# Optimization experiments

Hardware: AMD Instinct MI355X
Metric: run time of the kernel (lower is better)

Reference implementation:

```python
import jax, jax.numpy as jnp
import numpy as np
from jax import lax

START_IDX = 0
END_IDX = 1
NEG = -10000.0


def setup_inputs() -> dict:
    key = jax.random.key(0)
    k_h, k_t = jax.random.split(key)
    seq_len, tagset_size = 8192, 2048
    h = jax.random.normal(k_h, (seq_len, tagset_size), dtype=jnp.float32)
    transitions = jax.random.normal(k_t, (tagset_size, tagset_size), dtype=jnp.float32)
    # CRF constraints: nothing transitions FROM end into start row; nothing transitions TO end col
    transitions = transitions.at[START_IDX, :].set(NEG)
    transitions = transitions.at[:, END_IDX].set(NEG)
    return {"h": h, "transitions": transitions}


def reference(h, transitions):
    # h: [S, T] emission scores; transitions: [T, T], transitions[i, j] = score(j -> i)
    T = transitions.shape[0]
    init = jnp.full((T,), NEG, dtype=h.dtype).at[START_IDX].set(0.0)

    def step(forward_var, emit):
        # scores[i, j] = forward_var[j] + transitions[i, j] + emit[i]
        scores = forward_var[None, :] + transitions + emit[:, None]  # [T, T]
        return jax.nn.logsumexp(scores, axis=-1), None

    forward_var, _ = lax.scan(step, init, h)
    terminal = forward_var + transitions[END_IDX]
    return jax.nn.logsumexp(terminal)
```

## Files before the change

kernel.cpp:

```cpp
#include <hip/hip_runtime.h>


#define TSZ   2048
#define NCH   16
#define GBLK  16
#define NW    8
#define CH_LEN 512
#define BURN  24
#define START_I 0
#define END_I   1

typedef float v4f __attribute__((ext_vector_type(4)));
typedef _Float16 h2f __attribute__((ext_vector_type(2)));

__device__ __forceinline__ h2f pk16(float a, float b) {
    return __builtin_bit_cast(h2f, __builtin_amdgcn_cvt_pkrtz(a, b));
}
__device__ __forceinline__ void st_coh(float* p, float v) {
    asm volatile("global_store_dword %0, %1, off sc0 sc1"
                 :: "v"(p), "v"(v) : "memory");
}
__device__ __forceinline__ float ld_coh1(const float* p) {
    float r;
    asm volatile("global_load_dword %0, %1, off sc0 sc1\n\ts_waitcnt vmcnt(0)"
                 : "=&v"(r) : "v"(p) : "memory");
    return r;
}
__device__ __forceinline__ v4f ld_coh4(const float* p) {
    v4f r;
    asm volatile("global_load_dwordx4 %0, %1, off sc0 sc1\n\ts_waitcnt vmcnt(0)"
                 : "=&v"(r) : "v"(p) : "memory");
    return r;
}

__global__ __launch_bounds__(512, 1)
void crf_chain(const float* __restrict__ h, const float* __restrict__ tr,
               float* __restrict__ out, float* __restrict__ ws)
{
    const int tid  = threadIdx.x;
    const int lane = tid & 63;
    const int wv   = tid >> 6;
    const int blk  = blockIdx.x;
    const int c    = blk >> 4;
    const int b    = blk & (GBLK - 1);
    const int row_base = b * 128 + wv * 16;

    float* u_bufs = ws;
    float* usave  = ws + NCH * 2 * TSZ;
    float* ufin   = usave + NCH * TSZ;
    float* cbuf   = ufin + NCH * TSZ;
    int*   posts  = (int*)((char*)ws + 524544);

    __shared__ unsigned long long els64[32][512];
    __shared__ unsigned long long uh_sh[512];

    h2f e2r[12][16];
    #pragma unroll
    for (int r = 0; r < 12; ++r) {
        const float* trow = tr + (size_t)(row_base + r) * TSZ + 4 * lane;
        #pragma unroll
        for (int k = 0; k < 8; ++k) {
            float4 t4 = *(const float4*)(trow + 256 * k);
            e2r[r][2 * k]     = pk16(__expf(t4.x), __expf(t4.y));
            e2r[r][2 * k + 1] = pk16(__expf(t4.z), __expf(t4.w));
        }
    }
    #pragma unroll
    for (int rr = 0; rr < 4; ++rr) {
        const float* trow = tr + (size_t)(row_base + 12 + rr) * TSZ + 4 * lane;
        #pragma unroll
        for (int k = 0; k < 8; ++k) {
            float4 t4 = *(const float4*)(trow + 256 * k);
            unsigned lo = __builtin_bit_cast(unsigned, pk16(__expf(t4.x), __expf(t4.y)));
            unsigned hi = __builtin_bit_cast(unsigned, pk16(__expf(t4.z), __expf(t4.w)));
            els64[wv * 4 + rr][lane + 64 * k] =
                ((unsigned long long)hi << 32) | (unsigned long long)lo;
        }
    }

    const int s_keep  = c * CH_LEN;
    const int s_begin = (c == 0) ? 0 : (s_keep - BURN);
    const int s_end   = s_keep + CH_LEN;
    const int T_iter  = s_end - s_begin;

    const int q    = ((lane & 1) << 2) | (lane & 2) | ((lane >> 2) & 1);
    const int grow = row_base + q;

    if (tid < 128) {
        int row = b * 128 + tid;
        float v = (c == 0) ? ((row == START_I) ? 1.0f : 0.0f) : 1.0f;
        st_coh(&u_bufs[(c * 2 + 0) * TSZ + row], v);
    }
    __syncthreads();

    float Chat = 0.0f;

    for (int t = 0; t < T_iter; ++t) {
        const int s = s_begin + t;
        float* u_out = u_bufs + (c * 2 + ((t + 1) & 1)) * TSZ;
        const int out_neg = ((t + 1) >> 1) & 1;

        float hv0 = 0.0f, hv1 = 0.0f;
        if (lane < 8) {
            hv0 = h[(size_t)s * TSZ + grow];
            hv1 = h[(size_t)s * TSZ + grow + 8];
        }

        if (wv == 0) {
            const float* u_in = u_bufs + (c * 2 + (t & 1)) * TSZ;
            const int in_neg  = (t >> 1) & 1;

            v4f u0, u1, u2, u3, u4, u5, u6, u7;
            const float* pa = u_in + 4 * lane;
            const float* pb = pa + 1024;
            for (;;) {
                asm volatile(
                    "global_load_dwordx4 %0, %8, off sc0 sc1\n\t"
                    "global_load_dwordx4 %1, %8, off offset:1024 sc0 sc1\n\t"
                    "global_load_dwordx4 %2, %8, off offset:2048 sc0 sc1\n\t"
                    "global_load_dwordx4 %3, %8, off offset:3072 sc0 sc1\n\t"
                    "global_load_dwordx4 %4, %9, off sc0 sc1\n\t"
                    "global_load_dwordx4 %5, %9, off offset:1024 sc0 sc1\n\t"
                    "global_load_dwordx4 %6, %9, off offset:2048 sc0 sc1\n\t"
                    "global_load_dwordx4 %7, %9, off offset:3072 sc0 sc1\n\t"
                    "s_waitcnt vmcnt(0)"
                    : "=&v"(u0), "=&v"(u1), "=&v"(u2), "=&v"(u3),
                      "=&v"(u4), "=&v"(u5), "=&v"(u6), "=&v"(u7)
                    : "v"(pa), "v"(pb)
                    : "memory");
                bool fresh;
                if (in_neg) {
                    int a = __float_as_int(u0.x) & __float_as_int(u0.y) & __float_as_int(u0.z) & __float_as_int(u0.w);
                    a &= __float_as_int(u1.x) & __float_as_int(u1.y) & __float_as_int(u1.z) & __float_as_int(u1.w);
                    a &= __float_as_int(u2.x) & __float_as_int(u2.y) & __float_as_int(u2.z) & __float_as_int(u2.w);
                    a &= __float_as_int(u3.x) & __float_as_int(u3.y) & __float_as_int(u3.z) & __float_as_int(u3.w);
                    a &= __float_as_int(u4.x) & __float_as_int(u4.y) & __float_as_int(u4.z) & __float_as_int(u4.w);
                    a &= __float_as_int(u5.x) & __float_as_int(u5.y) & __float_as_int(u5.z) & __float_as_int(u5.w);
                    a &= __float_as_int(u6.x) & __float_as_int(u6.y) & __float_as_int(u6.z) & __float_as_int(u6.w);
                    a &= __float_as_int(u7.x) & __float_as_int(u7.y) & __float_as_int(u7.z) & __float_as_int(u7.w);
                    fresh = (a < 0);
                } else {
                    int o = __float_as_int(u0.x) | __float_as_int(u0.y) | __float_as_int(u0.z) | __float_as_int(u0.w);
                    o |= __float_as_int(u1.x) | __float_as_int(u1.y) | __float_as_int(u1.z) | __float_as_int(u1.w);
                    o |= __float_as_int(u2.x) | __float_as_int(u2.y) | __float_as_int(u2.z) | __float_as_int(u2.w);
                    o |= __float_as_int(u3.x) | __float_as_int(u3.y) | __float_as_int(u3.z) | __float_as_int(u3.w);
                    o |= __float_as_int(u4.x) | __float_as_int(u4.y) | __float_as_int(u4.z) | __float_as_int(u4.w);
                    o |= __float_as_int(u5.x) | __float_as_int(u5.y) | __float_as_int(u5.z) | __float_as_int(u5.w);
                    o |= __float_as_int(u6.x) | __float_as_int(u6.y) | __float_as_int(u6.z) | __float_as_int(u6.w);
                    o |= __float_as_int(u7.x) | __float_as_int(u7.y) | __float_as_int(u7.z) | __float_as_int(u7.w);
                    fresh = (o >= 0);
                }
                if (__all(fresh)) break;
            }

            float m;
            m =          fmaxf(fmaxf(fabsf(u0.x), fabsf(u0.y)), fmaxf(fabsf(u0.z), fabsf(u0.w)));
            m = fmaxf(m, fmaxf(fmaxf(fabsf(u1.x), fabsf(u1.y)), fmaxf(fabsf(u1.z), fabsf(u1.w))));
            m = fmaxf(m, fmaxf(fmaxf(fabsf(u2.x), fabsf(u2.y)), fmaxf(fabsf(u2.z), fabsf(u2.w))));
            m = fmaxf(m, fmaxf(fmaxf(fabsf(u3.x), fabsf(u3.y)), fmaxf(fabsf(u3.z), fabsf(u3.w))));
            m = fmaxf(m, fmaxf(fmaxf(fabsf(u4.x), fabsf(u4.y)), fmaxf(fabsf(u4.z), fabsf(u4.w))));
            m = fmaxf(m, fmaxf(fmaxf(fabsf(u5.x), fabsf(u5.y)), fmaxf(fabsf(u5.z), fabsf(u5.w))));
            m = fmaxf(m, fmaxf(fmaxf(fabsf(u6.x), fabsf(u6.y)), fmaxf(fabsf(u6.z), fabsf(u6.w))));
            m = fmaxf(m, fmaxf(fmaxf(fabsf(u7.x), fabsf(u7.y)), fmaxf(fabsf(u7.z), fabsf(u7.w))));
            #pragma unroll
            for (int d = 1; d < 64; d <<= 1) m = fmaxf(m, __shfl_xor(m, d, 64));

            const float rn = (in_neg ? -1.0f : 1.0f) / m;
            h2f uh[16];
            uh[0]  = pk16(u0.x * rn, u0.y * rn);  uh[1]  = pk16(u0.z * rn, u0.w * rn);
            uh[2]  = pk16(u1.x * rn, u1.y * rn);  uh[3]  = pk16(u1.z * rn, u1.w * rn);
            uh[4]  = pk16(u2.x * rn, u2.y * rn);  uh[5]  = pk16(u2.z * rn, u2.w * rn);
            uh[6]  = pk16(u3.x * rn, u3.y * rn);  uh[7]  = pk16(u3.z * rn, u3.w * rn);
            uh[8]  = pk16(u4.x * rn, u4.y * rn);  uh[9]  = pk16(u4.z * rn, u4.w * rn);
            uh[10] = pk16(u5.x * rn, u5.y * rn);  uh[11] = pk16(u5.z * rn, u5.w * rn);
            uh[12] = pk16(u6.x * rn, u6.y * rn);  uh[13] = pk16(u6.z * rn, u6.w * rn);
            uh[14] = pk16(u7.x * rn, u7.y * rn);  uh[15] = pk16(u7.z * rn, u7.w * rn);
            #pragma unroll
            for (int k = 0; k < 8; ++k) {
                unsigned long long qw =
                    ((unsigned long long)__builtin_bit_cast(unsigned, uh[2 * k + 1]) << 32) |
                    (unsigned long long)__builtin_bit_cast(unsigned, uh[2 * k]);
                uh_sh[lane + 64 * k] = qw;
            }

            if ((s + 1) > s_keep) Chat += __logf(m);
        }

        __syncthreads();

        h2f uh[16];
        #pragma unroll
        for (int k = 0; k < 8; ++k) {
            unsigned long long qw = uh_sh[lane + 64 * k];
            uh[2 * k]     = __builtin_bit_cast(h2f, (unsigned)qw);
            uh[2 * k + 1] = __builtin_bit_cast(h2f, (unsigned)(qw >> 32));
        }

        float acc[8];
        #pragma unroll
        for (int r = 0; r < 8; ++r) acc[r] = 0.0f;
        #pragma unroll
        for (int k = 0; k < 16; ++k) {
            #pragma unroll
            for (int r = 0; r < 8; ++r)
                acc[r] = __builtin_amdgcn_fdot2(e2r[r][k], uh[k], acc[r], false);
        }
        #pragma unroll
        for (int r = 0; r < 4; ++r) {
            float send = (lane & 1) ? acc[r] : acc[r + 4];
            float recv = __shfl_xor(send, 1, 64);
            float keep = (lane & 1) ? acc[r + 4] : acc[r];
            acc[r] = keep + recv;
        }
        #pragma unroll
        for (int r = 0; r < 2; ++r) {
            float send = (lane & 2) ? acc[r] : acc[r + 2];
            float recv = __shfl_xor(send, 2, 64);
            float keep = (lane & 2) ? acc[r + 2] : acc[r];
            acc[r] = keep + recv;
        }
        {
            float send = (lane & 4) ? acc[0] : acc[1];
            float recv = __shfl_xor(send, 4, 64);
            float keep = (lane & 4) ? acc[1] : acc[0];
            acc[0] = keep + recv;
        }
        acc[0] += __shfl_xor(acc[0], 8, 64);
        acc[0] += __shfl_xor(acc[0], 16, 64);
        acc[0] += __shfl_xor(acc[0], 32, 64);
        float resA = acc[0];

        #pragma unroll
        for (int r = 0; r < 8; ++r) acc[r] = 0.0f;
        #pragma unroll
        for (int k = 0; k < 8; ++k) {
            unsigned long long q0 = els64[wv * 4 + 0][lane + 64 * k];
            unsigned long long q1 = els64[wv * 4 + 1][lane + 64 * k];
            unsigned long long q2 = els64[wv * 4 + 2][lane + 64 * k];
            unsigned long long q3 = els64[wv * 4 + 3][lane + 64 * k];
            #pragma unroll
            for (int r = 0; r < 4; ++r) {
                acc[r] = __builtin_amdgcn_fdot2(e2r[8 + r][2 * k],     uh[2 * k],     acc[r], false);
                acc[r] = __builtin_amdgcn_fdot2(e2r[8 + r][2 * k + 1], uh[2 * k + 1], acc[r], false);
            }
            acc[4] = __builtin_amdgcn_fdot2(__builtin_bit_cast(h2f, (unsigned)q0),         uh[2 * k],     acc[4], false);
            acc[4] = __builtin_amdgcn_fdot2(__builtin_bit_cast(h2f, (unsigned)(q0 >> 32)), uh[2 * k + 1], acc[4], false);
            acc[5] = __builtin_amdgcn_fdot2(__builtin_bit_cast(h2f, (unsigned)q1),         uh[2 * k],     acc[5], false);
            acc[5] = __builtin_amdgcn_fdot2(__builtin_bit_cast(h2f, (unsigned)(q1 >> 32)), uh[2 * k + 1], acc[5], false);
            acc[6] = __builtin_amdgcn_fdot2(__builtin_bit_cast(h2f, (unsigned)q2),         uh[2 * k],     acc[6], false);
            acc[6] = __builtin_amdgcn_fdot2(__builtin_bit_cast(h2f, (unsigned)(q2 >> 32)), uh[2 * k + 1], acc[6], false);
            acc[7] = __builtin_amdgcn_fdot2(__builtin_bit_cast(h2f, (unsigned)q3),         uh[2 * k],     acc[7], false);
            acc[7] = __builtin_amdgcn_fdot2(__builtin_bit_cast(h2f, (unsigned)(q3 >> 32)), uh[2 * k + 1], acc[7], false);
        }
        #pragma unroll
        for (int r = 0; r < 4; ++r) {
            float send = (lane & 1) ? acc[r] : acc[r + 4];
            float recv = __shfl_xor(send, 1, 64);
            float keep = (lane & 1) ? acc[r + 4] : acc[r];
            acc[r] = keep + recv;
        }
        #pragma unroll
        for (int r = 0; r < 2; ++r) {
            float send = (lane & 2) ? acc[r] : acc[r + 2];
            float recv = __shfl_xor(send, 2, 64);
            float keep = (lane & 2) ? acc[r + 2] : acc[r];
            acc[r] = keep + recv;
        }
        {
            float send = (lane & 4) ? acc[0] : acc[1];
            float recv = __shfl_xor(send, 4, 64);
            float keep = (lane & 4) ? acc[1] : acc[0];
            acc[0] = keep + recv;
        }
        acc[0] += __shfl_xor(acc[0], 8, 64);
        acc[0] += __shfl_xor(acc[0], 16, 64);
        acc[0] += __shfl_xor(acc[0], 32, 64);
        float resB = acc[0];

        if (lane < 8) {
            float utA = resA * __expf(hv0);
            float utB = resB * __expf(hv1);
            st_coh(&u_out[grow],     out_neg ? -utA : utA);
            st_coh(&u_out[grow + 8], out_neg ? -utB : utB);
            if (c > 0 && (s + 1) == s_keep) {
                st_coh(&usave[c * TSZ + grow],     utA);
                st_coh(&usave[c * TSZ + grow + 8], utB);
            }
            if ((s + 1) == s_end) {
                st_coh(&ufin[c * TSZ + grow],     utA);
                st_coh(&ufin[c * TSZ + grow + 8], utB);
            }
        }
    }

    if (b == 0 && wv == 0 && lane == 0) st_coh(&cbuf[c], Chat);
    asm volatile("s_waitcnt vmcnt(0)" ::: "memory");
    if (lane == 0)
        __hip_atomic_store(&posts[blk * NW + wv], 1,
                           __ATOMIC_RELAXED, __HIP_MEMORY_SCOPE_AGENT);

    if (c == 0 && b == 0 && wv == 0) {
        int ok;
        do {
            __builtin_amdgcn_s_sleep(1);
            ok = 1;
            #pragma unroll
            for (int i = 0; i < 32; ++i) {
                int v = __hip_atomic_load(&posts[lane + 64 * i],
                                          __ATOMIC_RELAXED, __HIP_MEMORY_SCOPE_AGENT);
                ok &= (v == 1);
            }
        } while (!__all(ok));

        float O = 0.0f;
        for (int cc = 1; cc < NCH; ++cc) {
            float sa = 0.0f, sb = 0.0f;
            for (int j = 4 * lane; j < TSZ; j += 256) {
                v4f a4 = ld_coh4(&ufin[(cc - 1) * TSZ + j]);
                v4f b4 = ld_coh4(&usave[cc * TSZ + j]);
                sa += a4.x + a4.y + a4.z + a4.w;
                sb += b4.x + b4.y + b4.z + b4.w;
            }
            #pragma unroll
            for (int d = 1; d < 64; d <<= 1) {
                sa += __shfl_xor(sa, d, 64);
                sb += __shfl_xor(sb, d, 64);
            }
            O += ld_coh1(&cbuf[cc - 1]) + __logf(sa) - __logf(sb);
        }
        float se = 0.0f;
        for (int j = 4 * lane; j < TSZ; j += 256) {
            const float4 t4 = *(const float4*)(tr + (size_t)END_I * TSZ + j);
            v4f uf = ld_coh4(&ufin[(NCH - 1) * TSZ + j]);
            se += __expf(t4.x) * uf.x + __expf(t4.y) * uf.y +
                  __expf(t4.z) * uf.z + __expf(t4.w) * uf.w;
        }
        #pragma unroll
        for (int d = 1; d < 64; d <<= 1) se += __shfl_xor(se, d, 64);

        float ans = O + ld_coh1(&cbuf[NCH - 1]) + __logf(se);
        if (lane == 0) out[0] = ans;
    }
}

extern "C" void kernel_launch(void* const* d_in, const int* in_sizes, int n_in,
                              void* d_out, int out_size, void* d_ws, size_t ws_size,
                              hipStream_t stream) {
    const float* h  = (const float*)d_in[0];
    const float* tr = (const float*)d_in[1];
    (void)in_sizes; (void)n_in; (void)out_size; (void)ws_size;
    crf_chain<<<dim3(NCH * GBLK), dim3(512), 0, stream>>>(h, tr, (float*)d_out, (float*)d_ws);
}
```

Baseline: 2.227 ms.

## Interleave four sequence chunks per block group to hide inter-block polling latency

Splits the sequence into 64 chunks of 128 steps instead of 16 chunks of 512. Each group of 16 blocks now advances four chunks round-robin: it polls one chunk's state vector, packs another and runs the GEMV for a third in the same phase. The poll-and-normalize work is spread across all eight waves, with a shared-memory max reduction, instead of sitting on wave 0. The aim is to overlap the cross-block publish and poll latency of the serial recurrence with useful compute. In exchange it adds four times as many burn-in segments, more shared memory and more complex phase bookkeeping.

```diff
diff --git a/kernel.cpp b/kernel.cpp
--- a/kernel.cpp
+++ b/kernel.cpp
@@ -2,11 +2,12 @@
 
 
 #define TSZ   2048
-#define NCH   16
+#define NCH   64
 #define GBLK  16
 #define NW    8
-#define CH_LEN 512
+#define CH_LEN 128
 #define BURN  24
+#define TCYC  (CH_LEN + BURN)
 #define START_I 0
 #define END_I   1
 
@@ -41,7 +42,7 @@
     const int lane = tid & 63;
     const int wv   = tid >> 6;
     const int blk  = blockIdx.x;
-    const int c    = blk >> 4;
+    const int g    = blk >> 4;
     const int b    = blk & (GBLK - 1);
     const int row_base = b * 128 + wv * 16;
 
@@ -49,10 +50,11 @@
     float* usave  = ws + NCH * 2 * TSZ;
     float* ufin   = usave + NCH * TSZ;
     float* cbuf   = ufin + NCH * TSZ;
-    int*   posts  = (int*)((char*)ws + 524544);
+    int*   posts  = (int*)((char*)ws + 2097408);
 
     __shared__ unsigned long long els64[32][512];
-    __shared__ unsigned long long uh_sh[512];
+    __shared__ unsigned long long uh_sh[4][512];
+    __shared__ float smax_sh[4][8] __attribute__((aligned(16)));
 
     h2f e2r[12][16];
     #pragma unroll
@@ -78,124 +80,78 @@
         }
     }
 
-    const int s_keep  = c * CH_LEN;
-    const int s_begin = (c == 0) ? 0 : (s_keep - BURN);
-    const int s_end   = s_keep + CH_LEN;
-    const int T_iter  = s_end - s_begin;
+    const int ccs[4] = { g, 16 + g, 32 + g, 48 + g };
+    int s0s[4], sks[4], ses[4];
+    float* ubs[4];
+    #pragma unroll
+    for (int r = 0; r < 4; ++r) {
+        sks[r] = ccs[r] * CH_LEN;
+        ses[r] = sks[r] + CH_LEN;
+        s0s[r] = (ccs[r] == 0) ? 0 : (sks[r] - BURN);
+        ubs[r] = u_bufs + ccs[r] * 2 * TSZ;
+    }
 
     const int q    = ((lane & 1) << 2) | (lane & 2) | ((lane >> 2) & 1);
     const int grow = row_base + q;
 
     if (tid < 128) {
         int row = b * 128 + tid;
-        float v = (c == 0) ? ((row == START_I) ? 1.0f : 0.0f) : 1.0f;
-        st_coh(&u_bufs[(c * 2 + 0) * TSZ + row], v);
+        #pragma unroll
+        for (int r = 0; r < 4; ++r)
+            st_coh(&ubs[r][row],
+                   (ccs[r] == 0) ? ((row == START_I) ? 1.0f : 0.0f) : 1.0f);
     }
     __syncthreads();
 
-    float Chat = 0.0f;
-
-    for (int t = 0; t < T_iter; ++t) {
-        const int s = s_begin + t;
-        float* u_out = u_bufs + (c * 2 + ((t + 1) & 1)) * TSZ;
-        const int out_neg = ((t + 1) >> 1) & 1;
-
-        float hv0 = 0.0f, hv1 = 0.0f;
-        if (lane < 8) {
-            hv0 = h[(size_t)s * TSZ + grow];
-            hv1 = h[(size_t)s * TSZ + grow + 8];
-        }
-
-        if (wv == 0) {
-            const float* u_in = u_bufs + (c * 2 + (t & 1)) * TSZ;
-            const int in_neg  = (t >> 1) & 1;
-
-            v4f u0, u1, u2, u3, u4, u5, u6, u7;
-            const float* pa = u_in + 4 * lane;
-            const float* pb = pa + 1024;
-            for (;;) {
-                asm volatile(
-                    "global_load_dwordx4 %0, %8, off sc0 sc1\n\t"
-                    "global_load_dwordx4 %1, %8, off offset:1024 sc0 sc1\n\t"
-                    "global_load_dwordx4 %2, %8, off offset:2048 sc0 sc1\n\t"
-                    "global_load_dwordx4 %3, %8, off offset:3072 sc0 sc1\n\t"
-                    "global_load_dwordx4 %4, %9, off sc0 sc1\n\t"
-                    "global_load_dwordx4 %5, %9, off offset:1024 sc0 sc1\n\t"
-                    "global_load_dwordx4 %6, %9, off offset:2048 sc0 sc1\n\t"
-                    "global_load_dwordx4 %7, %9, off offset:3072 sc0 sc1\n\t"
-                    "s_waitcnt vmcnt(0)"
-                    : "=&v"(u0), "=&v"(u1), "=&v"(u2), "=&v"(u3),
-                      "=&v"(u4), "=&v"(u5), "=&v"(u6), "=&v"(u7)
-                    : "v"(pa), "v"(pb)
-                    : "memory");
-                bool fresh;
-                if (in_neg) {
-                    int a = __float_as_int(u0.x) & __float_as_int(u0.y) & __float_as_int(u0.z) & __float_as_int(u0.w);
-                    a &= __float_as_int(u1.x) & __float_as_int(u1.y) & __float_as_int(u1.z) & __float_as_int(u1.w);
-                    a &= __float_as_int(u2.x) & __float_as_int(u2.y) & __float_as_int(u2.z) & __float_as_int(u2.w);
-                    a &= __float_as_int(u3.x) & __float_as_int(u3.y) & __float_as_int(u3.z) & __float_as_int(u3.w);
-                    a &= __float_as_int(u4.x) & __float_as_int(u4.y) & __float_as_int(u4.z) & __float_as_int(u4.w);
-                    a &= __float_as_int(u5.x) & __float_as_int(u5.y) & __float_as_int(u5.z) & __float_as_int(u5.w);
-                    a &= __float_as_int(u6.x) & __float_as_int(u6.y) & __float_as_int(u6.z) & __float_as_int(u6.w);
-                    a &= __float_as_int(u7.x) & __float_as_int(u7.y) & __float_as_int(u7.z) & __float_as_int(u7.w);
-                    fresh = (a < 0);
-                } else {
-                    int o = __float_as_int(u0.x) | __float_as_int(u0.y) | __float_as_int(u0.z) | __float_as_int(u0.w);
-                    o |= __float_as_int(u1.x) | __float_as_int(u1.y) | __float_as_int(u1.z) | __float_as_int(u1.w);
-                    o |= __float_as_int(u2.x) | __float_as_int(u2.y) | __float_as_int(u2.z) | __float_as_int(u2.w);
-                    o |= __float_as_int(u3.x) | __float_as_int(u3.y) | __float_as_int(u3.z) | __float_as_int(u3.w);
-                    o |= __float_as_int(u4.x) | __float_as_int(u4.y) | __float_as_int(u4.z) | __float_as_int(u4.w);
-                    o |= __float_as_int(u5.x) | __float_as_int(u5.y) | __float_as_int(u5.z) | __float_as_int(u5.w);
-                    o |= __float_as_int(u6.x) | __float_as_int(u6.y) | __float_as_int(u6.z) | __float_as_int(u6.w);
-                    o |= __float_as_int(u7.x) | __float_as_int(u7.y) | __float_as_int(u7.z) | __float_as_int(u7.w);
-                    fresh = (o >= 0);
-                }
-                if (__all(fresh)) break;
-            }
-
-            float m;
-            m =          fmaxf(fmaxf(fabsf(u0.x), fabsf(u0.y)), fmaxf(fabsf(u0.z), fabsf(u0.w)));
-            m = fmaxf(m, fmaxf(fmaxf(fabsf(u1.x), fabsf(u1.y)), fmaxf(fabsf(u1.z), fabsf(u1.w))));
-            m = fmaxf(m, fmaxf(fmaxf(fabsf(u2.x), fabsf(u2.y)), fmaxf(fabsf(u2.z), fabsf(u2.w))));
-            m = fmaxf(m, fmaxf(fmaxf(fabsf(u3.x), fabsf(u3.y)), fmaxf(fabsf(u3.z), fabsf(u3.w))));
-            m = fmaxf(m, fmaxf(fmaxf(fabsf(u4.x), fabsf(u4.y)), fmaxf(fabsf(u4.z), fabsf(u4.w))));
-            m = fmaxf(m, fmaxf(fmaxf(fabsf(u5.x), fabsf(u5.y)), fmaxf(fabsf(u5.z), fabsf(u5.w))));
-            m = fmaxf(m, fmaxf(fmaxf(fabsf(u6.x), fabsf(u6.y)), fmaxf(fabsf(u6.z), fabsf(u6.w))));
-            m = fmaxf(m, fmaxf(fmaxf(fabsf(u7.x), fabsf(u7.y)), fmaxf(fabsf(u7.z), fabsf(u7.w))));
-            #pragma unroll
-            for (int d = 1; d < 64; d <<= 1) m = fmaxf(m, __shfl_xor(m, d, 64));
-
-            const float rn = (in_neg ? -1.0f : 1.0f) / m;
-            h2f uh[16];
-            uh[0]  = pk16(u0.x * rn, u0.y * rn);  uh[1]  = pk16(u0.z * rn, u0.w * rn);
-            uh[2]  = pk16(u1.x * rn, u1.y * rn);  uh[3]  = pk16(u1.z * rn, u1.w * rn);
-            uh[4]  = pk16(u2.x * rn, u2.y * rn);  uh[5]  = pk16(u2.z * rn, u2.w * rn);
-            uh[6]  = pk16(u3.x * rn, u3.y * rn);  uh[7]  = pk16(u3.z * rn, u3.w * rn);
-            uh[8]  = pk16(u4.x * rn, u4.y * rn);  uh[9]  = pk16(u4.z * rn, u4.w * rn);
-            uh[10] = pk16(u5.x * rn, u5.y * rn);  uh[11] = pk16(u5.z * rn, u5.w * rn);
-            uh[12] = pk16(u6.x * rn, u6.y * rn);  uh[13] = pk16(u6.z * rn, u6.w * rn);
-            uh[14] = pk16(u7.x * rn, u7.y * rn);  uh[15] = pk16(u7.z * rn, u7.w * rn);
-            #pragma unroll
-            for (int k = 0; k < 8; ++k) {
-                unsigned long long qw =
-                    ((unsigned long long)__builtin_bit_cast(unsigned, uh[2 * k + 1]) << 32) |
-                    (unsigned long long)__builtin_bit_cast(unsigned, uh[2 * k]);
-                uh_sh[lane + 64 * k] = qw;
-            }
-
-            if ((s + 1) > s_keep) Chat += __logf(m);
-        }
-
-        __syncthreads();
-
+    float Chat[4] = {0.0f, 0.0f, 0.0f, 0.0f};
+    v4f pu = {};
+
+    auto POLL_ISSUE = [&](const float* ubase, int par) -> v4f {
+        v4f r;
+        const float* p = ubase + par * TSZ + (wv << 8) + 4 * lane;
+        asm volatile("global_load_dwordx4 %0, %1, off sc0 sc1"
+                     : "=&v"(r) : "v"(p) : "memory");
+        return r;
+    };
+    auto POLL_FINISH = [&](v4f& pv, const float* ubase, int par, int in_neg, int cidx) {
+        const float* p = ubase + par * TSZ + (wv << 8) + 4 * lane;
+        asm volatile("s_waitcnt vmcnt(0)" : "+v"(pv) :: "memory");
+        for (;;) {
+            int a0 = __float_as_int(pv.x), a1 = __float_as_int(pv.y);
+            int a2 = __float_as_int(pv.z), a3 = __float_as_int(pv.w);
+            bool fresh = in_neg ? (((a0 & a1) & (a2 & a3)) < 0)
+                                : (((a0 | a1) | (a2 | a3)) >= 0);
+            if (__all(fresh)) break;
+            asm volatile("global_load_dwordx4 %0, %1, off sc0 sc1\n\ts_waitcnt vmcnt(0)"
+                         : "=&v"(pv) : "v"(p) : "memory");
+        }
+        float m = fmaxf(fmaxf(fabsf(pv.x), fabsf(pv.y)),
+                        fmaxf(fabsf(pv.z), fabsf(pv.w)));
+        #pragma unroll
+        for (int d = 1; d < 64; d <<= 1) m = fmaxf(m, __shfl_xor(m, d, 64));
+        if (lane == 0) smax_sh[cidx][wv] = m;
+    };
+    auto PACK = [&](v4f pv, int in_neg, bool kept, float& ch, int cidx) {
+        v4f m0 = *(const v4f*)&smax_sh[cidx][0];
+        v4f m1 = *(const v4f*)&smax_sh[cidx][4];
+        float gm = fmaxf(fmaxf(fmaxf(m0.x, m0.y), fmaxf(m0.z, m0.w)),
+                         fmaxf(fmaxf(m1.x, m1.y), fmaxf(m1.z, m1.w)));
+        float rn = (in_neg ? -1.0f : 1.0f) / gm;
+        unsigned lo = __builtin_bit_cast(unsigned, pk16(pv.x * rn, pv.y * rn));
+        unsigned hi = __builtin_bit_cast(unsigned, pk16(pv.z * rn, pv.w * rn));
+        uh_sh[cidx][lane + 64 * wv] =
+            ((unsigned long long)hi << 32) | (unsigned long long)lo;
+        if (kept) ch += __logf(gm);
+    };
+
+    auto GEMV_COMPUTE = [&](const unsigned long long* uh_src, float& outA, float& outB) {
         h2f uh[16];
         #pragma unroll
         for (int k = 0; k < 8; ++k) {
-            unsigned long long qw = uh_sh[lane + 64 * k];
+            unsigned long long qw = uh_src[lane + 64 * k];
             uh[2 * k]     = __builtin_bit_cast(h2f, (unsigned)qw);
             uh[2 * k + 1] = __builtin_bit_cast(h2f, (unsigned)(qw >> 32));
         }
-
         float acc[8];
         #pragma unroll
         for (int r = 0; r < 8; ++r) acc[r] = 0.0f;
@@ -228,7 +184,7 @@
         acc[0] += __shfl_xor(acc[0], 8, 64);
         acc[0] += __shfl_xor(acc[0], 16, 64);
         acc[0] += __shfl_xor(acc[0], 32, 64);
-        float resA = acc[0];
+        outA = acc[0];
 
         #pragma unroll
         for (int r = 0; r < 8; ++r) acc[r] = 0.0f;
@@ -275,31 +231,95 @@
         acc[0] += __shfl_xor(acc[0], 8, 64);
         acc[0] += __shfl_xor(acc[0], 16, 64);
         acc[0] += __shfl_xor(acc[0], 32, 64);
-        float resB = acc[0];
-
-        if (lane < 8) {
-            float utA = resA * __expf(hv0);
-            float utB = resB * __expf(hv1);
-            st_coh(&u_out[grow],     out_neg ? -utA : utA);
-            st_coh(&u_out[grow + 8], out_neg ? -utB : utB);
-            if (c > 0 && (s + 1) == s_keep) {
-                st_coh(&usave[c * TSZ + grow],     utA);
-                st_coh(&usave[c * TSZ + grow + 8], utB);
-            }
-            if ((s + 1) == s_end) {
-                st_coh(&ufin[c * TSZ + grow],     utA);
-                st_coh(&ufin[c * TSZ + grow + 8], utB);
-            }
-        }
-    }
-
-    if (b == 0 && wv == 0 && lane == 0) st_coh(&cbuf[c], Chat);
+        outB = acc[0];
+    };
+
+    auto BAR = [&]() {
+        __builtin_amdgcn_sched_barrier(0);
+        asm volatile("s_waitcnt lgkmcnt(0)" ::: "memory");
+        __builtin_amdgcn_s_barrier();
+        __builtin_amdgcn_sched_barrier(0);
+    };
+
+    {
+        v4f p0 = POLL_ISSUE(ubs[0], 0);
+        POLL_FINISH(p0, ubs[0], 0, 0, 0);
+        pu = p0;
+        BAR();
+    }
+    {
+        v4f p1 = POLL_ISSUE(ubs[1], 0);
+        const int spk = s0s[0];
+        PACK(pu, 0, (spk + 1 > sks[0]) && (spk + 1 <= ses[0]), Chat[0], 0);
+        POLL_FINISH(p1, ubs[1], 0, 0, 1);
+        pu = p1;
+        BAR();
+    }
+
+#define PHASE(T_, R_) do {                                                    \
+    constexpr int A_ = (R_) & 3;                                              \
+    constexpr int B_ = ((R_) + 1) & 3;                                        \
+    constexpr int C_ = ((R_) + 2) & 3;                                        \
+    const int tB_ = (B_ <= (R_)) ? (T_) + 1 : (T_);                           \
+    const int tC_ = (C_ <= (R_)) ? (T_) + 1 : (T_);                           \
+    const int sA_ = s0s[A_] + (T_);                                           \
+    float hA0_ = 0.0f, hA1_ = 0.0f;                                           \
+    if (lane < 8) {                                                           \
+        hA0_ = h[(size_t)sA_ * TSZ + grow];                                   \
+        hA1_ = h[(size_t)sA_ * TSZ + grow + 8];                               \
+    }                                                                         \
+    const bool doPoll_ = (tC_ < TCYC);                                        \
+    const bool doPack_ = (tB_ < TCYC);                                        \
+    v4f pnew_ = {};                                                           \
+    if (doPoll_) pnew_ = POLL_ISSUE(ubs[C_], tC_ & 1);                        \
+    if (doPack_) {                                                            \
+        const int spk_ = s0s[B_] + tB_;                                       \
+        PACK(pu, (tB_ >> 1) & 1,                                              \
+             (spk_ + 1 > sks[B_]) && (spk_ + 1 <= ses[B_]), Chat[B_], B_);    \
+    }                                                                         \
+    float resA_, resB_;                                                       \
+    GEMV_COMPUTE(&uh_sh[A_][0], resA_, resB_);                                \
+    if (doPoll_) POLL_FINISH(pnew_, ubs[C_], tC_ & 1, (tC_ >> 1) & 1, C_);    \
+    {                                                                         \
+        const int outp_ = ((T_) + 1) & 1, outn_ = (((T_) + 1) >> 1) & 1;      \
+        if (lane < 8) {                                                       \
+            float utA_ = resA_ * __expf(hA0_);                                \
+            float utB_ = resB_ * __expf(hA1_);                                \
+            float* uo_ = ubs[A_] + outp_ * TSZ;                               \
+            st_coh(&uo_[grow],     outn_ ? -utA_ : utA_);                     \
+            st_coh(&uo_[grow + 8], outn_ ? -utB_ : utB_);                     \
+            if (ccs[A_] > 0 && sA_ + 1 == sks[A_]) {                          \
+                st_coh(&usave[ccs[A_] * TSZ + grow],     utA_);               \
+                st_coh(&usave[ccs[A_] * TSZ + grow + 8], utB_);               \
+            }                                                                 \
+            if (sA_ + 1 == ses[A_]) {                                         \
+                st_coh(&ufin[ccs[A_] * TSZ + grow],     utA_);                \
+                st_coh(&ufin[ccs[A_] * TSZ + grow + 8], utB_);                \
+            }                                                                 \
+        }                                                                     \
+    }                                                                         \
+    if (doPoll_) pu = pnew_;                                                  \
+    BAR();                                                                    \
+} while (0)
+
+    for (int T = 0; T < TCYC; ++T) {
+        PHASE(T, 0);
+        PHASE(T, 1);
+        PHASE(T, 2);
+        PHASE(T, 3);
+    }
+#undef PHASE
+
+    if (b == 0 && wv == 0 && lane == 0) {
+        #pragma unroll
+        for (int r = 0; r < 4; ++r) st_coh(&cbuf[ccs[r]], Chat[r]);
+    }
     asm volatile("s_waitcnt vmcnt(0)" ::: "memory");
     if (lane == 0)
         __hip_atomic_store(&posts[blk * NW + wv], 1,
                            __ATOMIC_RELAXED, __HIP_MEMORY_SCOPE_AGENT);
 
-    if (c == 0 && b == 0 && wv == 0) {
+    if (blk == 0 && wv == 0) {
         int ok;
         do {
             __builtin_amdgcn_s_sleep(1);
@@ -349,5 +369,5 @@
     const float* h  = (const float*)d_in[0];
     const float* tr = (const float*)d_in[1];
     (void)in_sizes; (void)n_in; (void)out_size; (void)ws_size;
-    crf_chain<<<dim3(NCH * GBLK), dim3(512), 0, stream>>>(h, tr, (float*)d_out, (float*)d_ws);
-}
+    crf_chain<<<dim3(256), dim3(512), 0, stream>>>(h, tr, (float*)d_out, (float*)d_ws);
+}
```

Result: slower. 2.824 ms (+26.8%).
